# Kernel optimization log

Measured on AMD Instinct MI355X. Metric: run time of the kernel, lower is better.

## Reference

```python
import jax, jax.numpy as jnp
import numpy as np

HEADS = 8
KS = 7
PAD = 3


def grouped_conv1x1(x, w):
    # x: (B, Cin, H, W), w: (heads, Cout/h, Cin/h) -> (B, Cout, H, W)
    B, Cin, H, W = x.shape
    g, co, ci = w.shape
    xg = x.reshape(B, g, ci, H, W)
    out = jnp.einsum('bgchw,goc->bgohw', xg, w)
    return out.reshape(B, g * co, H, W)


def unfold2d(p, k):
    # p: (B, C, Hp, Wp) -> (B, C, H, W, k, k) sliding windows, stride 1
    B, C, Hp, Wp = p.shape
    H, W = Hp - k + 1, Wp - k + 1
    rows = [jnp.stack([p[:, :, i:i + H, j:j + W] for j in range(k)], axis=-1)
            for i in range(k)]
    return jnp.stack(rows, axis=-2)  # (B,C,H,W,k,k)


def setup_inputs() -> dict:
    key = jax.random.key(0)
    ks = jax.random.split(key, 7)
    B, Cin, H, W = 8, 64, 64, 64
    Cout = 64
    g = HEADS
    return {
        'x': jax.random.normal(ks[0], (B, Cin, H, W), jnp.float32),
        'r': jax.random.normal(ks[1], (1,), jnp.float32),
        'w_q': jax.random.normal(ks[2], (g, Cout // g, Cin // g), jnp.float32) * 0.2,
        'w_k': jax.random.normal(ks[3], (g, Cout // g, Cin // g), jnp.float32) * 0.2,
        'w_v': jax.random.normal(ks[4], (g, Cout // g, Cin // g), jnp.float32) * 0.2,
        'rel_h': jax.random.normal(ks[5], (Cout // 2, KS), jnp.float32),
        'rel_w': jax.random.normal(ks[6], (Cout // 2, KS), jnp.float32),
    }


def reference(x, r, w_q, w_k, w_v, rel_h, rel_w):
    B, Cin, H, W = x.shape
    g = HEADS
    Cout = w_q.shape[0] * w_q.shape[1]
    dh = Cout // g

    padded = jnp.pad(x, ((0, 0), (0, 0), (PAD, PAD), (PAD, PAD)))
    q = grouped_conv1x1(x, w_q)            # (B, Cout, H, W)
    k = grouped_conv1x1(padded, w_k)       # (B, Cout, H+2p, W+2p)
    v = grouped_conv1x1(padded, w_v)

    k = unfold2d(k, KS)                    # (B, Cout, H, W, KS, KS)
    v = unfold2d(v, KS)

    # learnable relative positional encoding: split channels in half,
    # add rel_h along window-height, rel_w along window-width
    half = Cout // 2
    k_h = k[:, :half] + rel_h[None, :, None, None, :, None]
    k_w = k[:, half:] + rel_w[None, :, None, None, None, :]
    k = jnp.concatenate([k_h, k_w], axis=1)

    K2 = KS * KS
    k = k.reshape(B, g, dh, H, W, K2)
    v = v.reshape(B, g, dh, H, W, K2)
    q = q.reshape(B, g, dh, H, W, 1)

    scale = np.sqrt(g / Cout).astype(np.float32)
    logits = (q * k).sum(axis=2, keepdims=True) * scale   # (B,g,1,H,W,K2)
    attn = jax.nn.softmax(logits, axis=-1)
    out = (attn * v).sum(axis=-1)                          # (B,g,dh,H,W)
    return out.reshape(B, Cout, H, W)
```

## Files before the change

### kernel.cpp

```cpp
#include <hip/hip_runtime.h>
#include <math.h>

#define NG  8
#define DH  8
#define NCP 4
#define KS  7
#define PAD 3
#define TH  16
#define TW  32
#define OW  2
#define TPH 22
#define RSTW 40
#define PLW  (TPH * RSTW)
#define CH  64
#define HH  64
#define WW  64

typedef __fp16 h2v __attribute__((ext_vector_type(2)));
typedef __fp16 h4v __attribute__((ext_vector_type(4)));

#if __has_builtin(__builtin_amdgcn_exp2f)
#define EXP2(x) __builtin_amdgcn_exp2f(x)
#else
#define EXP2(x) exp2f(x)
#endif

__device__ __forceinline__ int imin(int a, int b) { return a < b ? a : b; }
__device__ __forceinline__ int imax(int a, int b) { return a > b ? a : b; }

__global__ __launch_bounds__(256, 2)
void saconv_kernel(const float* __restrict__ x,
                   const float* __restrict__ wq,
                   const float* __restrict__ wk,
                   const float* __restrict__ wv,
                   const float* __restrict__ relh,
                   const float* __restrict__ relw,
                   float* __restrict__ out) {
  __shared__ h2v xs2[NCP * PLW];

  const int tx  = threadIdx.x;
  const int ty  = threadIdx.y;
  const int tid = ty * 16 + tx;
  const int bz  = blockIdx.z;
  const int b   = bz >> 3;
  const int g   = bz & 7;
  const int h0  = blockIdx.y * TH;
  const int w0  = blockIdx.x * TW;

  const float* xb = x + (size_t)(b * CH + g * DH) * (HH * WW);
  const int NCHK = NCP * TPH * 19;
  #pragma unroll
  for (int kk = 0; kk < 7; kk++) {
    int f = tid + kk * 256;
    if (f < NCHK) {
      int cp  = f / (TPH * 19);
      int r   = f - cp * (TPH * 19);
      int row = r / 19;
      int cc  = r - row * 19;
      int yy  = h0 + row - PAD;
      int cy  = imin(imax(yy, 0), HH - 1);
      bool yok = (yy >= 0) & (yy < HH);
      const float* p0 = xb + ((size_t)(2 * cp) * HH + cy) * WW;
      float v0[2], v1[2];
      #pragma unroll
      for (int e = 0; e < 2; e++) {
        int xx = w0 + 2 * cc + e - PAD;
        int cx = imin(imax(xx, 0), WW - 1);
        bool inb = yok & (xx >= 0) & (xx < WW);
        float a0 = p0[cx];
        float a1 = p0[HH * WW + cx];
        v0[e] = inb ? a0 : 0.0f;
        v1[e] = inb ? a1 : 0.0f;
      }
      h2v pk0 = __builtin_amdgcn_cvt_pkrtz(v0[0], v1[0]);
      h2v pk1 = __builtin_amdgcn_cvt_pkrtz(v0[1], v1[1]);
      h4v w4 = { pk0.x, pk0.y, pk1.x, pk1.y };
      *(h4v*)&xs2[cp * PLW + row * RSTW + 2 * cc] = w4;
    }
  }

  const float sl2e = 0.35355339059327373f * 1.4426950408889634f;
  h2v  qkh[OW][NCP];
  float rq[OW][KS];
  {
    float xc[OW][DH];
    const float* xq = xb + (size_t)(h0 + ty) * WW + (w0 + 2 * tx);
    #pragma unroll
    for (int o = 0; o < OW; o++)
      #pragma unroll
      for (int ci = 0; ci < DH; ci++)
        xc[o][ci] = xq[(size_t)ci * (HH * WW) + o];

    float q_[OW][DH];
    #pragma unroll
    for (int o = 0; o < OW; o++)
      #pragma unroll
      for (int c = 0; c < DH; c++) {
        float a = 0.f;
        #pragma unroll
        for (int ci = 0; ci < DH; ci++)
          a = fmaf(wq[(g * DH + c) * DH + ci], xc[o][ci], a);
        q_[o][c] = a;
      }
    #pragma unroll
    for (int o = 0; o < OW; o++)
      #pragma unroll
      for (int cp = 0; cp < NCP; cp++) {
        float a0 = 0.f, a1 = 0.f;
        #pragma unroll
        for (int c = 0; c < DH; c++) {
          a0 = fmaf(q_[o][c], wk[(g * DH + c) * DH + 2 * cp], a0);
          a1 = fmaf(q_[o][c], wk[(g * DH + c) * DH + 2 * cp + 1], a1);
        }
        qkh[o][cp] = __builtin_amdgcn_cvt_pkrtz(a0 * sl2e, a1 * sl2e);
      }
    if (g < 4) {
      #pragma unroll
      for (int o = 0; o < OW; o++)
        #pragma unroll
        for (int t = 0; t < KS; t++) {
          float a = 0.f;
          #pragma unroll
          for (int c = 0; c < DH; c++)
            a = fmaf(q_[o][c], relh[(g * DH + c) * KS + t], a);
          rq[o][t] = a * sl2e;
        }
    } else {
      #pragma unroll
      for (int o = 0; o < OW; o++)
        #pragma unroll
        for (int t = 0; t < KS; t++) {
          float a = 0.f;
          #pragma unroll
          for (int c = 0; c < DH; c++)
            a = fmaf(q_[o][c], relw[((g - 4) * DH + c) * KS + t], a);
          rq[o][t] = a * sl2e;
        }
    }
  }
  __syncthreads();

  float s[OW], xa[OW][DH];
  #pragma unroll
  for (int o = 0; o < OW; o++) {
    s[o] = 0.f;
    #pragma unroll
    for (int ci = 0; ci < DH; ci++) xa[o][ci] = 0.f;
  }

#define WINLOOP(DINIT)                                                         \
  _Pragma("unroll")                                                            \
  for (int i = 0; i < KS; i++) {                                               \
    const int wbase = (ty + i) * RSTW + 2 * tx;                                \
    h2v xw[NCP][8];                                                            \
    _Pragma("unroll")                                                          \
    for (int cp = 0; cp < NCP; cp++) {                                         \
      const h2v* bp = &xs2[cp * PLW + wbase];                                  \
      _Pragma("unroll")                                                        \
      for (int k = 0; k < 8; k++) xw[cp][k] = bp[k];                           \
    }                                                                          \
    _Pragma("unroll")                                                          \
    for (int o = 0; o < OW; o++) {                                             \
      float e[KS];                                                             \
      float se = 0.f;                                                          \
      _Pragma("unroll")                                                        \
      for (int j = 0; j < KS; j++) {                                           \
        float d = (DINIT);                                                     \
        _Pragma("unroll")                                                      \
        for (int cp = 0; cp < NCP; cp++)                                       \
          d = __builtin_amdgcn_fdot2(qkh[o][cp], xw[cp][o + j], d, false);     \
        e[j] = EXP2(d);                                                        \
        se += e[j];                                                            \
      }                                                                        \
      s[o] += se;                                                              \
      _Pragma("unroll")                                                        \
      for (int cp = 0; cp < NCP; cp++) {                                       \
        float a0 = xa[o][2 * cp];                                              \
        float a1 = xa[o][2 * cp + 1];                                          \
        _Pragma("unroll")                                                      \
        for (int j = 0; j < KS; j++) {                                         \
          a0 = fmaf(e[j], (float)xw[cp][o + j].x, a0);                         \
          a1 = fmaf(e[j], (float)xw[cp][o + j].y, a1);                         \
        }                                                                      \
        xa[o][2 * cp]     = a0;                                                \
        xa[o][2 * cp + 1] = a1;                                                \
      }                                                                        \
    }                                                                          \
  }

  if (g < 4) { WINLOOP(rq[o][i]) }
  else       { WINLOOP(rq[o][j]) }
#undef WINLOOP

  #pragma unroll
  for (int o = 0; o < OW; o++) {
    float inv = 1.0f / s[o];
    #pragma unroll
    for (int ci = 0; ci < DH; ci++) xa[o][ci] *= inv;
  }

  const int h = h0 + ty;
  const int wbase = w0 + 2 * tx;
  #pragma unroll
  for (int c = 0; c < DH; c++) {
    float a0 = 0.f, a1 = 0.f;
    #pragma unroll
    for (int ci = 0; ci < DH; ci++) {
      float wvv = wv[(g * DH + c) * DH + ci];
      a0 = fmaf(wvv, xa[0][ci], a0);
      a1 = fmaf(wvv, xa[1][ci], a1);
    }
    *(float2*)(&out[((size_t)(b * CH + g * DH + c) * HH + h) * WW + wbase]) =
        make_float2(a0, a1);
  }
}

extern "C" void kernel_launch(void* const* d_in, const int* in_sizes, int n_in,
                              void* d_out, int out_size, void* d_ws, size_t ws_size,
                              hipStream_t stream) {
  const float* x    = (const float*)d_in[0];
  const float* wq   = (const float*)d_in[2];
  const float* wk   = (const float*)d_in[3];
  const float* wv   = (const float*)d_in[4];
  const float* relh = (const float*)d_in[5];
  const float* relw = (const float*)d_in[6];
  float* out = (float*)d_out;

  const int B = in_sizes[0] / (CH * HH * WW);
  dim3 grid(WW / TW, HH / TH, B * NG);
  dim3 block(16, 16, 1);
  saconv_kernel<<<grid, block, 0, stream>>>(x, wq, wk, wv, relh, relw, out);
}
```

Measured before the change: 18.57 us.

## Stage packed fp16 weights in LDS and use fdot2 for projections

Weights for q, k, v and the relative-position tables are converted to packed fp16 pairs in shared memory by a few threads. The q/k/rel projections and the final v projection then use fdot2 instead of scalar fp32 FMAs. The centre pixel values now come from the already-staged LDS tile rather than a second round of global loads. Window loads are widened to 8-byte h4v reads. This cuts scalar-load and FMA work in the prologue and epilogue at the cost of extra fp16 rounding in q, qk and the attention output, and the sync now sits before the projection setup.

```diff
diff --git a/kernel.cpp b/kernel.cpp
--- a/kernel.cpp
+++ b/kernel.cpp
@@ -37,6 +37,10 @@
                    const float* __restrict__ relw,
                    float* __restrict__ out) {
   __shared__ h2v xs2[NCP * PLW];
+  __shared__ h2v swq2[DH * NCP];
+  __shared__ h2v swv2[DH * NCP];
+  __shared__ h2v swk2[DH * NCP];
+  __shared__ h2v srel2[KS * NCP];
 
   const int tx  = threadIdx.x;
   const int ty  = threadIdx.y;
@@ -46,6 +50,39 @@
   const int g   = bz & 7;
   const int h0  = blockIdx.y * TH;
   const int w0  = blockIdx.x * TW;
+
+  const float sl2e = 0.35355339059327373f * 1.4426950408889634f;
+
+  if (tid < 32) {
+    int c = tid >> 2, cp = tid & 3;
+    float a0 = wq[g * 64 + c * 8 + 2 * cp];
+    float a1 = wq[g * 64 + c * 8 + 2 * cp + 1];
+    swq2[tid] = __builtin_amdgcn_cvt_pkrtz(a0, a1);
+  } else if (tid < 64) {
+    int t2 = tid - 32;
+    int c = t2 >> 2, cp = t2 & 3;
+    float a0 = wv[g * 64 + c * 8 + 2 * cp];
+    float a1 = wv[g * 64 + c * 8 + 2 * cp + 1];
+    swv2[t2] = __builtin_amdgcn_cvt_pkrtz(a0, a1);
+  } else if (tid < 96) {
+    int t2 = tid - 64;
+    int ci = t2 >> 2, cP = t2 & 3;
+    float a0 = wk[g * 64 + (2 * cP) * 8 + ci] * sl2e;
+    float a1 = wk[g * 64 + (2 * cP + 1) * 8 + ci] * sl2e;
+    swk2[t2] = __builtin_amdgcn_cvt_pkrtz(a0, a1);
+  } else if (tid < 96 + KS * NCP) {
+    int t2 = tid - 96;
+    int t = t2 >> 2, cP = t2 & 3;
+    float a0, a1;
+    if (g < 4) {
+      a0 = relh[(g * 8 + 2 * cP) * KS + t];
+      a1 = relh[(g * 8 + 2 * cP + 1) * KS + t];
+    } else {
+      a0 = relw[((g - 4) * 8 + 2 * cP) * KS + t];
+      a1 = relw[((g - 4) * 8 + 2 * cP + 1) * KS + t];
+    }
+    srel2[t2] = __builtin_amdgcn_cvt_pkrtz(a0 * sl2e, a1 * sl2e);
+  }
 
   const float* xb = x + (size_t)(b * CH + g * DH) * (HH * WW);
   const int NCHK = NCP * TPH * 19;
@@ -78,67 +115,57 @@
       *(h4v*)&xs2[cp * PLW + row * RSTW + 2 * cc] = w4;
     }
   }
-
-  const float sl2e = 0.35355339059327373f * 1.4426950408889634f;
+  __syncthreads();
+
   h2v  qkh[OW][NCP];
   float rq[OW][KS];
   {
-    float xc[OW][DH];
-    const float* xq = xb + (size_t)(h0 + ty) * WW + (w0 + 2 * tx);
+    h2v xc2[OW][NCP];
     #pragma unroll
     for (int o = 0; o < OW; o++)
       #pragma unroll
-      for (int ci = 0; ci < DH; ci++)
-        xc[o][ci] = xq[(size_t)ci * (HH * WW) + o];
-
-    float q_[OW][DH];
-    #pragma unroll
-    for (int o = 0; o < OW; o++)
+      for (int cp = 0; cp < NCP; cp++)
+        xc2[o][cp] = xs2[cp * PLW + (ty + PAD) * RSTW + (2 * tx + o + PAD)];
+
+    #pragma unroll
+    for (int o = 0; o < OW; o++) {
+      float q_[DH];
       #pragma unroll
       for (int c = 0; c < DH; c++) {
         float a = 0.f;
         #pragma unroll
-        for (int ci = 0; ci < DH; ci++)
-          a = fmaf(wq[(g * DH + c) * DH + ci], xc[o][ci], a);
-        q_[o][c] = a;
-      }
-    #pragma unroll
-    for (int o = 0; o < OW; o++)
-      #pragma unroll
-      for (int cp = 0; cp < NCP; cp++) {
-        float a0 = 0.f, a1 = 0.f;
+        for (int cp = 0; cp < NCP; cp++)
+          a = __builtin_amdgcn_fdot2(swq2[c * 4 + cp], xc2[o][cp], a, false);
+        q_[c] = a;
+      }
+      h2v qp[NCP];
+      #pragma unroll
+      for (int cP = 0; cP < NCP; cP++)
+        qp[cP] = __builtin_amdgcn_cvt_pkrtz(q_[2 * cP], q_[2 * cP + 1]);
+
+      float qkt[DH];
+      #pragma unroll
+      for (int ci = 0; ci < DH; ci++) {
+        float a = 0.f;
         #pragma unroll
-        for (int c = 0; c < DH; c++) {
-          a0 = fmaf(q_[o][c], wk[(g * DH + c) * DH + 2 * cp], a0);
-          a1 = fmaf(q_[o][c], wk[(g * DH + c) * DH + 2 * cp + 1], a1);
-        }
-        qkh[o][cp] = __builtin_amdgcn_cvt_pkrtz(a0 * sl2e, a1 * sl2e);
-      }
-    if (g < 4) {
-      #pragma unroll
-      for (int o = 0; o < OW; o++)
+        for (int cP = 0; cP < NCP; cP++)
+          a = __builtin_amdgcn_fdot2(qp[cP], swk2[ci * 4 + cP], a, false);
+        qkt[ci] = a;
+      }
+      #pragma unroll
+      for (int cp = 0; cp < NCP; cp++)
+        qkh[o][cp] = __builtin_amdgcn_cvt_pkrtz(qkt[2 * cp], qkt[2 * cp + 1]);
+
+      #pragma unroll
+      for (int t = 0; t < KS; t++) {
+        float a = 0.f;
         #pragma unroll
-        for (int t = 0; t < KS; t++) {
-          float a = 0.f;
-          #pragma unroll
-          for (int c = 0; c < DH; c++)
-            a = fmaf(q_[o][c], relh[(g * DH + c) * KS + t], a);
-          rq[o][t] = a * sl2e;
-        }
-    } else {
-      #pragma unroll
-      for (int o = 0; o < OW; o++)
-        #pragma unroll
-        for (int t = 0; t < KS; t++) {
-          float a = 0.f;
-          #pragma unroll
-          for (int c = 0; c < DH; c++)
-            a = fmaf(q_[o][c], relw[((g - 4) * DH + c) * KS + t], a);
-          rq[o][t] = a * sl2e;
-        }
-    }
-  }
-  __syncthreads();
+        for (int cP = 0; cP < NCP; cP++)
+          a = __builtin_amdgcn_fdot2(qp[cP], srel2[t * 4 + cP], a, false);
+        rq[o][t] = a;
+      }
+    }
+  }
 
   float s[OW], xa[OW][DH];
   #pragma unroll
@@ -155,9 +182,16 @@
     h2v xw[NCP][8];                                                            \
     _Pragma("unroll")                                                          \
     for (int cp = 0; cp < NCP; cp++) {                                         \
-      const h2v* bp = &xs2[cp * PLW + wbase];                                  \
-      _Pragma("unroll")                                                        \
-      for (int k = 0; k < 8; k++) xw[cp][k] = bp[k];                           \
+      const h4v* bp = (const h4v*)&xs2[cp * PLW + wbase];                      \
+      h4v r0 = bp[0], r1 = bp[1], r2 = bp[2], r3 = bp[3];                      \
+      xw[cp][0] = __builtin_shufflevector(r0, r0, 0, 1);                       \
+      xw[cp][1] = __builtin_shufflevector(r0, r0, 2, 3);                       \
+      xw[cp][2] = __builtin_shufflevector(r1, r1, 0, 1);                       \
+      xw[cp][3] = __builtin_shufflevector(r1, r1, 2, 3);                       \
+      xw[cp][4] = __builtin_shufflevector(r2, r2, 0, 1);                       \
+      xw[cp][5] = __builtin_shufflevector(r2, r2, 2, 3);                       \
+      xw[cp][6] = __builtin_shufflevector(r3, r3, 0, 1);                       \
+      xw[cp][7] = __builtin_shufflevector(r3, r3, 2, 3);                       \
     }                                                                          \
     _Pragma("unroll")                                                          \
     for (int o = 0; o < OW; o++) {                                             \
@@ -192,11 +226,14 @@
   else       { WINLOOP(rq[o][j]) }
 #undef WINLOOP
 
+  h2v xav2[OW][NCP];
   #pragma unroll
   for (int o = 0; o < OW; o++) {
     float inv = 1.0f / s[o];
     #pragma unroll
-    for (int ci = 0; ci < DH; ci++) xa[o][ci] *= inv;
+    for (int cp = 0; cp < NCP; cp++)
+      xav2[o][cp] = __builtin_amdgcn_cvt_pkrtz(xa[o][2 * cp] * inv,
+                                               xa[o][2 * cp + 1] * inv);
   }
 
   const int h = h0 + ty;
@@ -205,10 +242,9 @@
   for (int c = 0; c < DH; c++) {
     float a0 = 0.f, a1 = 0.f;
     #pragma unroll
-    for (int ci = 0; ci < DH; ci++) {
-      float wvv = wv[(g * DH + c) * DH + ci];
-      a0 = fmaf(wvv, xa[0][ci], a0);
-      a1 = fmaf(wvv, xa[1][ci], a1);
+    for (int cp = 0; cp < NCP; cp++) {
+      a0 = __builtin_amdgcn_fdot2(swv2[c * 4 + cp], xav2[0][cp], a0, false);
+      a1 = __builtin_amdgcn_fdot2(swv2[c * 4 + cp], xav2[1][cp], a1, false);
     }
     *(float2*)(&out[((size_t)(b * CH + g * DH + c) * HH + h) * WW + wbase]) =
         make_float2(a0, a1);
```

Measured after the change: 17.45 us. -6.0%, faster.
